# Optimization experiments

Hardware: AMD Instinct MI355X
Metric: run time of the kernel (lower is better)

The kernel has to match this reference:

```python
import jax, jax.numpy as jnp
import numpy as np

K = 3          # kernel_size
PAD = 1        # padding
FOCAL = 50.0
DMIN = 1.0
DMAX = 50.0
ORIG_H = 512.0  # original_image_size[1]


def setup_inputs() -> dict:
    key = jax.random.key(0)
    k1, k2 = jax.random.split(key)
    x = jax.random.normal(k1, (4, 64, 256, 256), dtype=jnp.float32)
    # conv weight [out_ch, in_ch, K, K] (bias=False)
    W = jax.random.normal(k2, (64, 64, K, K), dtype=jnp.float32) * 0.05
    return {"x": x, "W": W}


def _bilinear(img, xs, ys):
    """Bilinear sample img [B,C,H,W] at float pixel coords xs, ys [B,Ho,Wo].
    Zero padding outside the image (grid_sample semantics)."""
    B, C, H, Wd = img.shape
    Ho, Wo = xs.shape[1], xs.shape[2]
    x0 = jnp.floor(xs); y0 = jnp.floor(ys)
    wx1 = xs - x0; wx0 = 1.0 - wx1
    wy1 = ys - y0; wy0 = 1.0 - wy1
    img_flat = img.reshape(B, C, H * Wd)

    def gat(ix, iy):
        ixi = ix.astype(jnp.int32); iyi = iy.astype(jnp.int32)
        valid = (ixi >= 0) & (ixi < Wd) & (iyi >= 0) & (iyi < H)
        idx = jnp.clip(iyi, 0, H - 1) * Wd + jnp.clip(ixi, 0, Wd - 1)
        v = jnp.take_along_axis(img_flat, idx.reshape(B, 1, Ho * Wo), axis=2)
        v = v.reshape(B, C, Ho, Wo)
        return v * valid[:, None].astype(img.dtype)

    return (gat(x0, y0) * (wx0 * wy0)[:, None]
            + gat(x0 + 1, y0) * (wx1 * wy0)[:, None]
            + gat(x0, y0 + 1) * (wx0 * wy1)[:, None]
            + gat(x0 + 1, y0 + 1) * (wx1 * wy1)[:, None])


def reference(x, W):
    B, C, H, Wd = x.shape
    downsample = ORIG_H / H  # 2.0 for H=256

    # upper branch: plain 3x3 conv, padding 1, no bias
    x_upper = jax.lax.conv_general_dilated(x, W, (1, 1), [(PAD, PAD), (PAD, PAD)])

    # geometry -> clamped depth (geometry_method='max', formulation='depth')
    depth = jnp.clip(jnp.max(x, axis=1), DMIN, DMAX)  # [B,H,W]

    # Frontal homography: Hom01 = I with [1,2] = focal/(downsample*depth);
    # its inverse Hom10 shifts y by -s.
    s = FOCAL / (downsample * depth)  # [B,H,W]

    xi = jnp.arange(Wd, dtype=x.dtype)[None, None, :]
    yi = jnp.arange(H, dtype=x.dtype)[None, :, None]
    xs = jnp.broadcast_to(xi, (B, H, Wd))
    ys = yi - s  # Hom10 applied to pixel coords

    # warp input with per-pixel Hom10 (pass_warped_images=True)
    x2 = _bilinear(x, xs, ys)

    # deformable conv: per-pixel offset from Hom10 is (dx,dy)=(0,-s) for all 9 taps
    x_lower = jnp.zeros_like(x_upper)
    for ky in range(K):
        for kx in range(K):
            sx = xs + (kx - PAD)
            sy = ys + (ky - PAD)
            tap = _bilinear(x2, sx, sy)  # [B,C,H,W]
            x_lower = x_lower + jnp.einsum('bchw,oc->bohw', tap, W[:, :, ky, kx])

    # project with 'min' over the stacked (upper, lower) branches
    return jnp.minimum(x_upper, x_lower)
```

## Files before the change

### kernel.cpp

```cpp
#include <hip/hip_runtime.h>
#include <cmath>

constexpr int BB = 4, CC = 64, HH = 256, WW = 256;
constexpr int WP = 258;
constexpr int C2R = 257;

typedef short short8 __attribute__((ext_vector_type(8)));
typedef float f32x4 __attribute__((ext_vector_type(4)));
#define MFMA_BF16 __builtin_amdgcn_mfma_f32_16x16x32_bf16

union U16x8 { uint4 v; unsigned short h[8]; };
union U16x4 { uint2 v; unsigned short h[4]; };

__device__ inline unsigned short f2bf(float f) {
  unsigned u = __builtin_bit_cast(unsigned, f);
  u += 0x7fffu + ((u >> 16) & 1u);
  return (unsigned short)(u >> 16);
}
__device__ inline unsigned short f2bf_trunc(float f) {
  return (unsigned short)(__builtin_bit_cast(unsigned, f) >> 16);
}
__device__ inline float bf2f(unsigned short h) {
  unsigned u = ((unsigned)h) << 16;
  return __builtin_bit_cast(float, u);
}

__global__ __launch_bounds__(256, 2) void k_pack(const float* __restrict__ x,
                                                 float* __restrict__ s,
                                                 unsigned short* __restrict__ xn) {
  __shared__ float tile[CC * 257];
  const int t = threadIdx.x, y = blockIdx.x, b = blockIdx.y;
  const float* base = x + (size_t)b * CC * HH * WW + y * WW + t;
  float m = -1e30f;
#pragma unroll 8
  for (int c = 0; c < CC; ++c) {
    float v = base[(size_t)c * HH * WW];
    tile[c * 257 + t] = v;
    m = fmaxf(m, v);
  }
  s[(b * HH + y) * WW + t] = 25.0f / fminf(fmaxf(m, 1.0f), 50.0f);
  uint4* xn4 = (uint4*)xn;
  if (t < 16) {
    int col = (t >> 3) ? (WP - 1) : 0, c8 = t & 7;
    xn4[(((size_t)(b * HH + y) * WP + col) * CC + c8 * 8) >> 3] =
        make_uint4(0, 0, 0, 0);
  }
  __syncthreads();
#pragma unroll
  for (int g = 0; g < 8; ++g) {
    int px = g * 32 + (t >> 3), c8 = t & 7;
    U16x8 r;
#pragma unroll
    for (int j = 0; j < 8; ++j) r.h[j] = f2bf(tile[(c8 * 8 + j) * 257 + px]);
    xn4[(((size_t)(b * HH + y) * WP + px + 1) * CC + c8 * 8) >> 3] = r.v;
  }
}

__global__ __launch_bounds__(256) void k_wpack(const float* __restrict__ Wt,
                                               unsigned short* __restrict__ Wp) {
  int gid = blockIdx.x * 256 + threadIdx.x;
  int lane = gid & 63, kc = (gid >> 6) & 1, mt = (gid >> 7) & 3, tap = gid >> 9;
  int o = mt * 16 + (lane & 15);
  int kb = kc * 32 + (lane >> 4) * 8;
  int ky = tap / 3, kx = tap % 3;
  U16x8 r;
#pragma unroll
  for (int j = 0; j < 8; ++j)
    r.h[j] = f2bf(Wt[o * 576 + (kb + j) * 9 + ky * 3 + kx]);
  ((uint4*)Wp)[gid] = r.v;
}

#define STAGE_TILE(src4, rowBase, colBase, bb)                                 \
  do {                                                                         \
    for (int i = 0; i < 13; ++i) {                                             \
      int idx = i * 256 + t;                                                   \
      if (idx < 3168) {                                                        \
        int rr_ = idx / 528, rem = idx % 528;                                  \
        int col_ = rem >> 3, ch_ = rem & 7;                                    \
        int xrow = (rowBase) + rr_;                                            \
        uint4 v = make_uint4(0, 0, 0, 0);                                      \
        if (xrow >= 0 && xrow < HH)                                            \
          v = src4[((size_t)((bb)*HH + xrow) * WP + (colBase) + col_) * 8 + ch_]; \
        lds[(rr_ * 66 + col_) * 8 + (ch_ ^ (col_ & 7))] = v;                   \
      }                                                                        \
    }                                                                          \
  } while (0)

__global__ __launch_bounds__(256, 2) void k_lower(const unsigned short* __restrict__ xn,
                                                  const unsigned short* __restrict__ Wp,
                                                  const float* __restrict__ s,
                                                  unsigned short* __restrict__ c2) {
  __shared__ uint4 lds[3168];
  const int t = threadIdx.x;
  const int ctile = blockIdx.x & 3, tr = blockIdx.x >> 2;
  const int b = blockIdx.y;
  const int r0 = tr * 4 - 1;
  const int colBase = ctile * 64;

  const uint4* xn4 = (const uint4*)xn;
  for (int i = 0; i < 13; ++i) {
    int idx = i * 256 + t;
    if (idx < 3168) {
      int rr_ = idx / 528, rem = idx % 528;
      int col_ = rem >> 3, ch_ = rem & 7;
      int xrow = r0 - 1 + rr_;
      uint4 v = make_uint4(0, 0, 0, 0);
      if (xrow >= 0 && xrow < HH) {
        int px = colBase + col_ - 1;
        int pxc = min(max(px, 0), WW - 1);
        float sv = s[(b * HH + xrow) * WW + pxc];
        float ys = (float)xrow - sv;
        float fy = floorf(ys);
        float wfr = ys - fy;
        int i0 = (int)fy;
        float w0 = (i0 >= 0) ? 1.0f - wfr : 0.0f;
        float w1 = (i0 + 1 >= 0) ? wfr : 0.0f;
        int a0 = max(i0, 0), a1 = max(i0 + 1, 0);
        U16x8 u0, u1, rr;
        u0.v = xn4[((size_t)(b * HH + a0) * WP + colBase + col_) * 8 + ch_];
        u1.v = xn4[((size_t)(b * HH + a1) * WP + colBase + col_) * 8 + ch_];
#pragma unroll
        for (int k = 0; k < 8; ++k)
          rr.h[k] = f2bf_trunc(w0 * bf2f(u0.h[k]) + w1 * bf2f(u1.h[k]));
        v = rr.v;
      }
      lds[(rr_ * 66 + col_) * 8 + (ch_ ^ (col_ & 7))] = v;
    }
  }

  const int lane = t & 63, w = t >> 6;
  const int ow = w & 1, rg = w >> 1, lr = rg * 2;
  const int quad = lane >> 4, l15 = lane & 15;

  short8 wf[9][2][2];
  const uint4* wp4 = (const uint4*)Wp;
#pragma unroll
  for (int tap = 0; tap < 9; ++tap)
#pragma unroll
    for (int ct = 0; ct < 2; ++ct)
#pragma unroll
      for (int kc = 0; kc < 2; ++kc)
        wf[tap][ct][kc] = __builtin_bit_cast(
            short8, wp4[((tap * 4 + (ow * 2 + ct)) * 2 + kc) * 64 + lane]);
  __syncthreads();

#pragma unroll 1
  for (int pt = 0; pt < 4; ++pt) {
    f32x4 acc[2][2] = {{{0.f, 0.f, 0.f, 0.f}, {0.f, 0.f, 0.f, 0.f}},
                       {{0.f, 0.f, 0.f, 0.f}, {0.f, 0.f, 0.f, 0.f}}};
#pragma unroll
    for (int ir = 0; ir < 4; ++ir) {
      int ldr = lr + ir;
#pragma unroll
      for (int kx = 0; kx < 3; ++kx) {
        int col = pt * 16 + l15 + kx;
        int cb = (ldr * 66 + col) * 8, sw = col & 7;
#pragma unroll
        for (int kc = 0; kc < 2; ++kc) {
          short8 xf = __builtin_bit_cast(short8, lds[cb + ((kc * 4 + quad) ^ sw)]);
          if (ir <= 2) {
#pragma unroll
            for (int ct = 0; ct < 2; ++ct)
              acc[0][ct] = MFMA_BF16(wf[ir * 3 + kx][ct][kc], xf, acc[0][ct], 0, 0, 0);
          }
          if (ir >= 1) {
#pragma unroll
            for (int ct = 0; ct < 2; ++ct)
              acc[1][ct] = MFMA_BF16(wf[(ir - 1) * 3 + kx][ct][kc], xf, acc[1][ct], 0, 0, 0);
          }
        }
      }
    }
#pragma unroll
    for (int rr = 0; rr < 2; ++rr) {
      int r = r0 + lr + rr;
      if (r > 255) continue;
      int px = colBase + pt * 16 + l15;
#pragma unroll
      for (int ct = 0; ct < 2; ++ct) {
        f32x4 A = acc[rr][ct];
        int ch = (ow * 2 + ct) * 16 + quad * 4;
        unsigned short h0 = f2bf(A[0]), h1 = f2bf(A[1]), h2 = f2bf(A[2]), h3 = f2bf(A[3]);
        uint2 val = make_uint2((unsigned)h0 | ((unsigned)h1 << 16),
                               (unsigned)h2 | ((unsigned)h3 << 16));
        *(uint2*)(c2 + (((size_t)(b * C2R + (r + 1)) * WW + px) * CC + ch)) = val;
      }
    }
  }
}

__global__ __launch_bounds__(256, 2) void k_final(const unsigned short* __restrict__ xn,
                                                  const unsigned short* __restrict__ Wp,
                                                  const float* __restrict__ s,
                                                  const unsigned short* __restrict__ c2,
                                                  float* __restrict__ out) {
  __shared__ uint4 lds[3168];
  const int t = threadIdx.x;
  const int ctile = blockIdx.x & 3, tr = blockIdx.x >> 2;
  const int b = blockIdx.y;
  const int y0 = tr * 4;
  const int colBase = ctile * 64;

  const uint4* src4 = (const uint4*)xn;
  STAGE_TILE(src4, y0 - 1, colBase, b);

  const int lane = t & 63, w = t >> 6;
  const int ow = w & 1, rg = w >> 1, lr = rg * 2;
  const int quad = lane >> 4, l15 = lane & 15;

  short8 wf[9][2][2];
  const uint4* wp4 = (const uint4*)Wp;
#pragma unroll
  for (int tap = 0; tap < 9; ++tap)
#pragma unroll
    for (int ct = 0; ct < 2; ++ct)
#pragma unroll
      for (int kc = 0; kc < 2; ++kc)
        wf[tap][ct][kc] = __builtin_bit_cast(
            short8, wp4[((tap * 4 + (ow * 2 + ct)) * 2 + kc) * 64 + lane]);
  __syncthreads();

#pragma unroll 1
  for (int pt = 0; pt < 4; ++pt) {
    f32x4 acc[2][2] = {{{0.f, 0.f, 0.f, 0.f}, {0.f, 0.f, 0.f, 0.f}},
                       {{0.f, 0.f, 0.f, 0.f}, {0.f, 0.f, 0.f, 0.f}}};
#pragma unroll
    for (int ir = 0; ir < 4; ++ir) {
      int ldr = lr + ir;
#pragma unroll
      for (int kx = 0; kx < 3; ++kx) {
        int col = pt * 16 + l15 + kx;
        int cb = (ldr * 66 + col) * 8, sw = col & 7;
#pragma unroll
        for (int kc = 0; kc < 2; ++kc) {
          short8 xf = __builtin_bit_cast(short8, lds[cb + ((kc * 4 + quad) ^ sw)]);
          if (ir <= 2) {
#pragma unroll
            for (int ct = 0; ct < 2; ++ct)
              acc[0][ct] = MFMA_BF16(wf[ir * 3 + kx][ct][kc], xf, acc[0][ct], 0, 0, 0);
          }
          if (ir >= 1) {
#pragma unroll
            for (int ct = 0; ct < 2; ++ct)
              acc[1][ct] = MFMA_BF16(wf[(ir - 1) * 3 + kx][ct][kc], xf, acc[1][ct], 0, 0, 0);
          }
        }
      }
    }
    int px = colBase + pt * 16 + l15;
#pragma unroll
    for (int rr = 0; rr < 2; ++rr) {
      int y = y0 + lr + rr;
      float sv = s[(b * HH + y) * WW + px];
      float ys = (float)y - sv;
      float fy = floorf(ys);
      float wfr = ys - fy;
      int i0 = (int)fy;
      float lw0 = (i0 + 1 >= 0 && i0 + 1 <= HH) ? 1.0f - wfr : 0.0f;
      float lw1 = (i0 + 2 >= 0 && i0 + 2 <= HH) ? wfr : 0.0f;
      int a0 = min(max(i0 + 1, 0), HH);
      int a1 = min(max(i0 + 2, 0), HH);
#pragma unroll
      for (int ct = 0; ct < 2; ++ct) {
        f32x4 A = acc[rr][ct];
        int ch = (ow * 2 + ct) * 16 + quad * 4;
        U16x4 v0, v1;
        v0.v = *(const uint2*)(c2 + ((size_t)(b * C2R + a0) * WW + px) * CC + ch);
        v1.v = *(const uint2*)(c2 + ((size_t)(b * C2R + a1) * WW + px) * CC + ch);
#pragma unroll
        for (int reg = 0; reg < 4; ++reg) {
          float lower = lw0 * bf2f(v0.h[reg]) + lw1 * bf2f(v1.h[reg]);
          out[((size_t)(b * CC + ch + reg) * HH + y) * WW + px] =
              fminf(A[reg], lower);
        }
      }
    }
  }
}

extern "C" void kernel_launch(void* const* d_in, const int* in_sizes, int n_in,
                              void* d_out, int out_size, void* d_ws, size_t ws_size,
                              hipStream_t stream) {
  const float* x = (const float*)d_in[0];
  const float* Wt = (const float*)d_in[1];
  float* out = (float*)d_out;

  char* ws = (char*)d_ws;
  float* s = (float*)ws;
  unsigned short* Wp = (unsigned short*)(ws + 1048576);
  unsigned short* xn = (unsigned short*)(ws + 1122304);
  unsigned short* c2 = (unsigned short*)(ws + 34938880);
  k_pack<<<dim3(HH, BB), 256, 0, stream>>>(x, s, xn);
  k_wpack<<<dim3(18), 256, 0, stream>>>(Wt, Wp);
  k_lower<<<dim3(4 * 65, BB), 256, 0, stream>>>(xn, Wp, s, c2);
  k_final<<<dim3(4 * 64, BB), 256, 0, stream>>>(xn, Wp, s, c2, out);
}
```

Before: 197.2 us.

## Split pack by half-rows, restructure conv loops to cut registers and raise occupancy

```diff
diff --git a/kernel.cpp b/kernel.cpp
--- a/kernel.cpp
+++ b/kernel.cpp
@@ -25,34 +25,45 @@
   return __builtin_bit_cast(float, u);
 }
 
-__global__ __launch_bounds__(256, 2) void k_pack(const float* __restrict__ x,
+__global__ __launch_bounds__(256, 4) void k_pack(const float* __restrict__ x,
                                                  float* __restrict__ s,
                                                  unsigned short* __restrict__ xn) {
-  __shared__ float tile[CC * 257];
-  const int t = threadIdx.x, y = blockIdx.x, b = blockIdx.y;
-  const float* base = x + (size_t)b * CC * HH * WW + y * WW + t;
+  __shared__ float tile[CC * 129];
+  __shared__ float pmax[2][128];
+  const int t = threadIdx.x;
+  const int half = blockIdx.x & 1, y = blockIdx.x >> 1, b = blockIdx.y;
+  const int px0 = half * 128;
+  const int pxl = t & 127, chb = (t >> 7) * 32;
+
+  const float* base = x + (size_t)b * CC * HH * WW + (size_t)y * WW + px0 + pxl;
   float m = -1e30f;
 #pragma unroll 8
-  for (int c = 0; c < CC; ++c) {
-    float v = base[(size_t)c * HH * WW];
-    tile[c * 257 + t] = v;
+  for (int i = 0; i < 32; ++i) {
+    float v = base[(size_t)(chb + i) * HH * WW];
+    tile[(chb + i) * 129 + pxl] = v;
     m = fmaxf(m, v);
   }
-  s[(b * HH + y) * WW + t] = 25.0f / fminf(fmaxf(m, 1.0f), 50.0f);
+  pmax[t >> 7][pxl] = m;
+
   uint4* xn4 = (uint4*)xn;
-  if (t < 16) {
-    int col = (t >> 3) ? (WP - 1) : 0, c8 = t & 7;
-    xn4[(((size_t)(b * HH + y) * WP + col) * CC + c8 * 8) >> 3] =
+  if (t < 8) {
+    int col = half ? (WP - 1) : 0;
+    xn4[(((size_t)(b * HH + y) * WP + col) * CC + t * 8) >> 3] =
         make_uint4(0, 0, 0, 0);
   }
   __syncthreads();
-#pragma unroll
-  for (int g = 0; g < 8; ++g) {
+
+  if (t < 128) {
+    float mm = fmaxf(pmax[0][t], pmax[1][t]);
+    s[(b * HH + y) * WW + px0 + t] = 25.0f / fminf(fmaxf(mm, 1.0f), 50.0f);
+  }
+#pragma unroll
+  for (int g = 0; g < 4; ++g) {
     int px = g * 32 + (t >> 3), c8 = t & 7;
     U16x8 r;
 #pragma unroll
-    for (int j = 0; j < 8; ++j) r.h[j] = f2bf(tile[(c8 * 8 + j) * 257 + px]);
-    xn4[(((size_t)(b * HH + y) * WP + px + 1) * CC + c8 * 8) >> 3] = r.v;
+    for (int j = 0; j < 8; ++j) r.h[j] = f2bf(tile[(c8 * 8 + j) * 129 + px]);
+    xn4[(((size_t)(b * HH + y) * WP + px0 + px + 1) * CC + c8 * 8) >> 3] = r.v;
   }
 }
 
@@ -70,23 +81,7 @@
   ((uint4*)Wp)[gid] = r.v;
 }
 
-#define STAGE_TILE(src4, rowBase, colBase, bb)                                 \
-  do {                                                                         \
-    for (int i = 0; i < 13; ++i) {                                             \
-      int idx = i * 256 + t;                                                   \
-      if (idx < 3168) {                                                        \
-        int rr_ = idx / 528, rem = idx % 528;                                  \
-        int col_ = rem >> 3, ch_ = rem & 7;                                    \
-        int xrow = (rowBase) + rr_;                                            \
-        uint4 v = make_uint4(0, 0, 0, 0);                                      \
-        if (xrow >= 0 && xrow < HH)                                            \
-          v = src4[((size_t)((bb)*HH + xrow) * WP + (colBase) + col_) * 8 + ch_]; \
-        lds[(rr_ * 66 + col_) * 8 + (ch_ ^ (col_ & 7))] = v;                   \
-      }                                                                        \
-    }                                                                          \
-  } while (0)
-
-__global__ __launch_bounds__(256, 2) void k_lower(const unsigned short* __restrict__ xn,
+__global__ __launch_bounds__(256, 3) void k_lower(const unsigned short* __restrict__ xn,
                                                   const unsigned short* __restrict__ Wp,
                                                   const float* __restrict__ s,
                                                   unsigned short* __restrict__ c2) {
@@ -98,98 +93,120 @@
   const int colBase = ctile * 64;
 
   const uint4* xn4 = (const uint4*)xn;
+  float w0a[13], w1a[13];
+  int o0a[13], o1a[13], la[13];
+  bool act[13], va[13];
+#pragma unroll
   for (int i = 0; i < 13; ++i) {
     int idx = i * 256 + t;
-    if (idx < 3168) {
-      int rr_ = idx / 528, rem = idx % 528;
-      int col_ = rem >> 3, ch_ = rem & 7;
-      int xrow = r0 - 1 + rr_;
+    act[i] = (idx < 3168);
+    int rr_ = idx / 528, rem = idx % 528;
+    int col_ = rem >> 3, ch_ = rem & 7;
+    int xrow = r0 - 1 + rr_;
+    va[i] = act[i] && (xrow >= 0) && (xrow < HH);
+    la[i] = (rr_ * 66 + col_) * 8 + (ch_ ^ (col_ & 7));
+    float sv = 0.0f;
+    int pxc = min(max(colBase + col_ - 1, 0), WW - 1);
+    if (va[i]) sv = s[(b * HH + xrow) * WW + pxc];
+    float ys = (float)xrow - sv;
+    float fy = floorf(ys);
+    float wfr = ys - fy;
+    int i0 = (int)fy;
+    w0a[i] = (i0 >= 0) ? 1.0f - wfr : 0.0f;
+    w1a[i] = (i0 + 1 >= 0) ? wfr : 0.0f;
+    int a0 = max(i0, 0), a1 = max(i0 + 1, 0);
+    o0a[i] = ((b * HH + a0) * WP + colBase + col_) * 8 + ch_;
+    o1a[i] = ((b * HH + a1) * WP + colBase + col_) * 8 + ch_;
+  }
+#pragma unroll
+  for (int i = 0; i < 13; ++i) {
+    if (act[i]) {
       uint4 v = make_uint4(0, 0, 0, 0);
-      if (xrow >= 0 && xrow < HH) {
-        int px = colBase + col_ - 1;
-        int pxc = min(max(px, 0), WW - 1);
-        float sv = s[(b * HH + xrow) * WW + pxc];
-        float ys = (float)xrow - sv;
-        float fy = floorf(ys);
-        float wfr = ys - fy;
-        int i0 = (int)fy;
-        float w0 = (i0 >= 0) ? 1.0f - wfr : 0.0f;
-        float w1 = (i0 + 1 >= 0) ? wfr : 0.0f;
-        int a0 = max(i0, 0), a1 = max(i0 + 1, 0);
+      if (va[i]) {
         U16x8 u0, u1, rr;
-        u0.v = xn4[((size_t)(b * HH + a0) * WP + colBase + col_) * 8 + ch_];
-        u1.v = xn4[((size_t)(b * HH + a1) * WP + colBase + col_) * 8 + ch_];
+        u0.v = xn4[o0a[i]];
+        u1.v = xn4[o1a[i]];
 #pragma unroll
         for (int k = 0; k < 8; ++k)
-          rr.h[k] = f2bf_trunc(w0 * bf2f(u0.h[k]) + w1 * bf2f(u1.h[k]));
+          rr.h[k] = f2bf_trunc(w0a[i] * bf2f(u0.h[k]) + w1a[i] * bf2f(u1.h[k]));
         v = rr.v;
       }
-      lds[(rr_ * 66 + col_) * 8 + (ch_ ^ (col_ & 7))] = v;
+      lds[la[i]] = v;
     }
   }
 
   const int lane = t & 63, w = t >> 6;
   const int ow = w & 1, rg = w >> 1, lr = rg * 2;
   const int quad = lane >> 4, l15 = lane & 15;
-
-  short8 wf[9][2][2];
   const uint4* wp4 = (const uint4*)Wp;
-#pragma unroll
-  for (int tap = 0; tap < 9; ++tap)
-#pragma unroll
-    for (int ct = 0; ct < 2; ++ct)
-#pragma unroll
-      for (int kc = 0; kc < 2; ++kc)
-        wf[tap][ct][kc] = __builtin_bit_cast(
-            short8, wp4[((tap * 4 + (ow * 2 + ct)) * 2 + kc) * 64 + lane]);
   __syncthreads();
 
 #pragma unroll 1
-  for (int pt = 0; pt < 4; ++pt) {
-    f32x4 acc[2][2] = {{{0.f, 0.f, 0.f, 0.f}, {0.f, 0.f, 0.f, 0.f}},
-                       {{0.f, 0.f, 0.f, 0.f}, {0.f, 0.f, 0.f, 0.f}}};
-#pragma unroll
-    for (int ir = 0; ir < 4; ++ir) {
-      int ldr = lr + ir;
-#pragma unroll
-      for (int kx = 0; kx < 3; ++kx) {
-        int col = pt * 16 + l15 + kx;
-        int cb = (ldr * 66 + col) * 8, sw = col & 7;
-#pragma unroll
-        for (int kc = 0; kc < 2; ++kc) {
-          short8 xf = __builtin_bit_cast(short8, lds[cb + ((kc * 4 + quad) ^ sw)]);
-          if (ir <= 2) {
-#pragma unroll
-            for (int ct = 0; ct < 2; ++ct)
-              acc[0][ct] = MFMA_BF16(wf[ir * 3 + kx][ct][kc], xf, acc[0][ct], 0, 0, 0);
-          }
-          if (ir >= 1) {
-#pragma unroll
-            for (int ct = 0; ct < 2; ++ct)
-              acc[1][ct] = MFMA_BF16(wf[(ir - 1) * 3 + kx][ct][kc], xf, acc[1][ct], 0, 0, 0);
+  for (int pp = 0; pp < 2; ++pp) {
+    f32x4 acc[2][2][2];
+#pragma unroll
+    for (int pi = 0; pi < 2; ++pi)
+#pragma unroll
+      for (int rr = 0; rr < 2; ++rr)
+#pragma unroll
+        for (int ct = 0; ct < 2; ++ct) acc[pi][rr][ct] = {0.f, 0.f, 0.f, 0.f};
+
+#pragma unroll 1
+    for (int kc = 0; kc < 2; ++kc) {
+      short8 wf[9][2];
+#pragma unroll
+      for (int tap = 0; tap < 9; ++tap)
+#pragma unroll
+        for (int ct = 0; ct < 2; ++ct)
+          wf[tap][ct] = __builtin_bit_cast(
+              short8, wp4[((tap * 4 + (ow * 2 + ct)) * 2 + kc) * 64 + lane]);
+#pragma unroll
+      for (int pi = 0; pi < 2; ++pi) {
+        int pt = pp * 2 + pi;
+#pragma unroll
+        for (int ir = 0; ir < 4; ++ir) {
+          int ldr = lr + ir;
+#pragma unroll
+          for (int kx = 0; kx < 3; ++kx) {
+            int col = pt * 16 + l15 + kx;
+            short8 xf = __builtin_bit_cast(
+                short8, lds[(ldr * 66 + col) * 8 + ((kc * 4 + quad) ^ (col & 7))]);
+            if (ir <= 2) {
+#pragma unroll
+              for (int ct = 0; ct < 2; ++ct)
+                acc[pi][0][ct] = MFMA_BF16(wf[ir * 3 + kx][ct], xf, acc[pi][0][ct], 0, 0, 0);
+            }
+            if (ir >= 1) {
+#pragma unroll
+              for (int ct = 0; ct < 2; ++ct)
+                acc[pi][1][ct] = MFMA_BF16(wf[(ir - 1) * 3 + kx][ct], xf, acc[pi][1][ct], 0, 0, 0);
+            }
           }
         }
       }
     }
 #pragma unroll
-    for (int rr = 0; rr < 2; ++rr) {
-      int r = r0 + lr + rr;
-      if (r > 255) continue;
-      int px = colBase + pt * 16 + l15;
-#pragma unroll
-      for (int ct = 0; ct < 2; ++ct) {
-        f32x4 A = acc[rr][ct];
-        int ch = (ow * 2 + ct) * 16 + quad * 4;
-        unsigned short h0 = f2bf(A[0]), h1 = f2bf(A[1]), h2 = f2bf(A[2]), h3 = f2bf(A[3]);
-        uint2 val = make_uint2((unsigned)h0 | ((unsigned)h1 << 16),
-                               (unsigned)h2 | ((unsigned)h3 << 16));
-        *(uint2*)(c2 + (((size_t)(b * C2R + (r + 1)) * WW + px) * CC + ch)) = val;
-      }
-    }
-  }
-}
-
-__global__ __launch_bounds__(256, 2) void k_final(const unsigned short* __restrict__ xn,
+    for (int pi = 0; pi < 2; ++pi) {
+      int px = colBase + (pp * 2 + pi) * 16 + l15;
+#pragma unroll
+      for (int rr = 0; rr < 2; ++rr) {
+        int r = r0 + lr + rr;
+        if (r > 255) continue;
+#pragma unroll
+        for (int ct = 0; ct < 2; ++ct) {
+          f32x4 A = acc[pi][rr][ct];
+          int ch = (ow * 2 + ct) * 16 + quad * 4;
+          unsigned short h0 = f2bf(A[0]), h1 = f2bf(A[1]), h2 = f2bf(A[2]), h3 = f2bf(A[3]);
+          uint2 val = make_uint2((unsigned)h0 | ((unsigned)h1 << 16),
+                                 (unsigned)h2 | ((unsigned)h3 << 16));
+          *(uint2*)(c2 + (((size_t)(b * C2R + (r + 1)) * WW + px) * CC + ch)) = val;
+        }
+      }
+    }
+  }
+}
+
+__global__ __launch_bounds__(256, 3) void k_final(const unsigned short* __restrict__ xn,
                                                   const unsigned short* __restrict__ Wp,
                                                   const float* __restrict__ s,
                                                   const unsigned short* __restrict__ c2,
@@ -202,76 +219,98 @@
   const int colBase = ctile * 64;
 
   const uint4* src4 = (const uint4*)xn;
-  STAGE_TILE(src4, y0 - 1, colBase, b);
+#pragma unroll
+  for (int i = 0; i < 13; ++i) {
+    int idx = i * 256 + t;
+    if (idx < 3168) {
+      int rr_ = idx / 528, rem = idx % 528;
+      int col_ = rem >> 3, ch_ = rem & 7;
+      int xrow = y0 - 1 + rr_;
+      uint4 v = make_uint4(0, 0, 0, 0);
+      if (xrow >= 0 && xrow < HH)
+        v = src4[((size_t)(b * HH + xrow) * WP + colBase + col_) * 8 + ch_];
+      lds[(rr_ * 66 + col_) * 8 + (ch_ ^ (col_ & 7))] = v;
+    }
+  }
 
   const int lane = t & 63, w = t >> 6;
   const int ow = w & 1, rg = w >> 1, lr = rg * 2;
   const int quad = lane >> 4, l15 = lane & 15;
-
-  short8 wf[9][2][2];
   const uint4* wp4 = (const uint4*)Wp;
-#pragma unroll
-  for (int tap = 0; tap < 9; ++tap)
-#pragma unroll
-    for (int ct = 0; ct < 2; ++ct)
-#pragma unroll
-      for (int kc = 0; kc < 2; ++kc)
-        wf[tap][ct][kc] = __builtin_bit_cast(
-            short8, wp4[((tap * 4 + (ow * 2 + ct)) * 2 + kc) * 64 + lane]);
   __syncthreads();
 
 #pragma unroll 1
-  for (int pt = 0; pt < 4; ++pt) {
-    f32x4 acc[2][2] = {{{0.f, 0.f, 0.f, 0.f}, {0.f, 0.f, 0.f, 0.f}},
-                       {{0.f, 0.f, 0.f, 0.f}, {0.f, 0.f, 0.f, 0.f}}};
-#pragma unroll
-    for (int ir = 0; ir < 4; ++ir) {
-      int ldr = lr + ir;
-#pragma unroll
-      for (int kx = 0; kx < 3; ++kx) {
-        int col = pt * 16 + l15 + kx;
-        int cb = (ldr * 66 + col) * 8, sw = col & 7;
-#pragma unroll
-        for (int kc = 0; kc < 2; ++kc) {
-          short8 xf = __builtin_bit_cast(short8, lds[cb + ((kc * 4 + quad) ^ sw)]);
-          if (ir <= 2) {
-#pragma unroll
-            for (int ct = 0; ct < 2; ++ct)
-              acc[0][ct] = MFMA_BF16(wf[ir * 3 + kx][ct][kc], xf, acc[0][ct], 0, 0, 0);
-          }
-          if (ir >= 1) {
-#pragma unroll
-            for (int ct = 0; ct < 2; ++ct)
-              acc[1][ct] = MFMA_BF16(wf[(ir - 1) * 3 + kx][ct][kc], xf, acc[1][ct], 0, 0, 0);
+  for (int pp = 0; pp < 2; ++pp) {
+    f32x4 acc[2][2][2];
+#pragma unroll
+    for (int pi = 0; pi < 2; ++pi)
+#pragma unroll
+      for (int rr = 0; rr < 2; ++rr)
+#pragma unroll
+        for (int ct = 0; ct < 2; ++ct) acc[pi][rr][ct] = {0.f, 0.f, 0.f, 0.f};
+
+#pragma unroll 1
+    for (int kc = 0; kc < 2; ++kc) {
+      short8 wf[9][2];
+#pragma unroll
+      for (int tap = 0; tap < 9; ++tap)
+#pragma unroll
+        for (int ct = 0; ct < 2; ++ct)
+          wf[tap][ct] = __builtin_bit_cast(
+              short8, wp4[((tap * 4 + (ow * 2 + ct)) * 2 + kc) * 64 + lane]);
+#pragma unroll
+      for (int pi = 0; pi < 2; ++pi) {
+        int pt = pp * 2 + pi;
+#pragma unroll
+        for (int ir = 0; ir < 4; ++ir) {
+          int ldr = lr + ir;
+#pragma unroll
+          for (int kx = 0; kx < 3; ++kx) {
+            int col = pt * 16 + l15 + kx;
+            short8 xf = __builtin_bit_cast(
+                short8, lds[(ldr * 66 + col) * 8 + ((kc * 4 + quad) ^ (col & 7))]);
+            if (ir <= 2) {
+#pragma unroll
+              for (int ct = 0; ct < 2; ++ct)
+                acc[pi][0][ct] = MFMA_BF16(wf[ir * 3 + kx][ct], xf, acc[pi][0][ct], 0, 0, 0);
+            }
+            if (ir >= 1) {
+#pragma unroll
+              for (int ct = 0; ct < 2; ++ct)
+                acc[pi][1][ct] = MFMA_BF16(wf[(ir - 1) * 3 + kx][ct], xf, acc[pi][1][ct], 0, 0, 0);
+            }
           }
         }
       }
     }
-    int px = colBase + pt * 16 + l15;
-#pragma unroll
-    for (int rr = 0; rr < 2; ++rr) {
-      int y = y0 + lr + rr;
-      float sv = s[(b * HH + y) * WW + px];
-      float ys = (float)y - sv;
-      float fy = floorf(ys);
-      float wfr = ys - fy;
-      int i0 = (int)fy;
-      float lw0 = (i0 + 1 >= 0 && i0 + 1 <= HH) ? 1.0f - wfr : 0.0f;
-      float lw1 = (i0 + 2 >= 0 && i0 + 2 <= HH) ? wfr : 0.0f;
-      int a0 = min(max(i0 + 1, 0), HH);
-      int a1 = min(max(i0 + 2, 0), HH);
-#pragma unroll
-      for (int ct = 0; ct < 2; ++ct) {
-        f32x4 A = acc[rr][ct];
-        int ch = (ow * 2 + ct) * 16 + quad * 4;
-        U16x4 v0, v1;
-        v0.v = *(const uint2*)(c2 + ((size_t)(b * C2R + a0) * WW + px) * CC + ch);
-        v1.v = *(const uint2*)(c2 + ((size_t)(b * C2R + a1) * WW + px) * CC + ch);
-#pragma unroll
-        for (int reg = 0; reg < 4; ++reg) {
-          float lower = lw0 * bf2f(v0.h[reg]) + lw1 * bf2f(v1.h[reg]);
-          out[((size_t)(b * CC + ch + reg) * HH + y) * WW + px] =
-              fminf(A[reg], lower);
+#pragma unroll
+    for (int pi = 0; pi < 2; ++pi) {
+      int px = colBase + (pp * 2 + pi) * 16 + l15;
+#pragma unroll
+      for (int rr = 0; rr < 2; ++rr) {
+        int y = y0 + lr + rr;
+        float sv = s[(b * HH + y) * WW + px];
+        float ys = (float)y - sv;
+        float fy = floorf(ys);
+        float wfr = ys - fy;
+        int i0 = (int)fy;
+        float lw0 = (i0 + 1 >= 0 && i0 + 1 <= HH) ? 1.0f - wfr : 0.0f;
+        float lw1 = (i0 + 2 >= 0 && i0 + 2 <= HH) ? wfr : 0.0f;
+        int a0 = min(max(i0 + 1, 0), HH);
+        int a1 = min(max(i0 + 2, 0), HH);
+#pragma unroll
+        for (int ct = 0; ct < 2; ++ct) {
+          f32x4 A = acc[pi][rr][ct];
+          int ch = (ow * 2 + ct) * 16 + quad * 4;
+          U16x4 v0, v1;
+          v0.v = *(const uint2*)(c2 + ((size_t)(b * C2R + a0) * WW + px) * CC + ch);
+          v1.v = *(const uint2*)(c2 + ((size_t)(b * C2R + a1) * WW + px) * CC + ch);
+#pragma unroll
+          for (int reg = 0; reg < 4; ++reg) {
+            float lower = lw0 * bf2f(v0.h[reg]) + lw1 * bf2f(v1.h[reg]);
+            out[((size_t)(b * CC + ch + reg) * HH + y) * WW + px] =
+                fminf(A[reg], lower);
+          }
         }
       }
     }
@@ -290,7 +329,7 @@
   unsigned short* Wp = (unsigned short*)(ws + 1048576);
   unsigned short* xn = (unsigned short*)(ws + 1122304);
   unsigned short* c2 = (unsigned short*)(ws + 34938880);
-  k_pack<<<dim3(HH, BB), 256, 0, stream>>>(x, s, xn);
+  k_pack<<<dim3(HH * 2, BB), 256, 0, stream>>>(x, s, xn);
   k_wpack<<<dim3(18), 256, 0, stream>>>(Wt, Wp);
   k_lower<<<dim3(4 * 65, BB), 256, 0, stream>>>(xn, Wp, s, c2);
   k_final<<<dim3(4 * 64, BB), 256, 0, stream>>>(xn, Wp, s, c2, out);
```

New measurement: 195.4 us. Within noise of the previous version (-0.9%).
